# Kernel optimization log

Measured on AMD Instinct MI355X. Metric: run time of the kernel, lower is better.

The kernel has to match this reference:

```python
import jax, jax.numpy as jnp
import numpy as np

N, E, D_IN, H, Z = 50000, 800000, 256, 96, 32
NEG_SLOPE = 0.2  # PyG GATConv default
BN_EPS = 1e-5


def _gat(x, src, dst, W, a, b, n):
    """Single-head GATConv (PyG semantics, self-loops already in src/dst)."""
    h = x @ W                                   # [N, F']
    e = jax.nn.leaky_relu((h @ a[0])[src] + (h @ a[1])[dst], NEG_SLOPE)  # [E]
    m = jax.ops.segment_max(e, dst, num_segments=n)
    ex = jnp.exp(e - m[dst])
    s = jax.ops.segment_sum(ex, dst, num_segments=n)
    alpha = ex / s[dst]                         # softmax over incoming edges
    out = jax.ops.segment_sum(alpha[:, None] * h[src], dst, num_segments=n)
    return out + b


def _bn(x, g, b):
    # BatchNorm1d in training mode: biased batch stats over nodes
    mu = jnp.mean(x, axis=0)
    v = jnp.var(x, axis=0)
    return g * (x - mu) / jnp.sqrt(v + BN_EPS) + b


def setup_inputs() -> dict:
    key = jax.random.key(0)
    ks = jax.random.split(key, 32)
    inp = {}
    inp["x"] = jax.random.normal(ks[0], (N, D_IN), jnp.float32)
    inp["edge_index"] = jax.random.randint(ks[1], (2, E), 0, N)
    inp["eps"] = jax.random.normal(ks[2], (N, Z), jnp.float32)

    def xav(k, di, do):
        s = float(np.sqrt(2.0 / (di + do)))
        return jax.random.normal(k, (di, do), jnp.float32) * s

    layers = [("enc1", D_IN, H), ("enc2", H, H), ("mu", H, Z), ("lv", H, Z),
              ("dec1", Z, H), ("dec2", H, H), ("out", H, D_IN)]
    ki = 3
    for nm, di, do in layers:
        inp[nm + "_W"] = xav(ks[ki], di, do)
        inp[nm + "_a"] = jax.random.normal(ks[ki + 1], (2, do), jnp.float32) * 0.1
        inp[nm + "_b"] = jnp.zeros((do,), jnp.float32)
        ki += 2
    for nm in ["bne1", "bne2", "bnd1", "bnd2"]:
        inp[nm + "_g"] = jnp.ones((H,), jnp.float32)
        inp[nm + "_b"] = jnp.zeros((H,), jnp.float32)
    return inp


def reference(x, edge_index, eps,
              enc1_W, enc1_a, enc1_b, enc2_W, enc2_a, enc2_b,
              mu_W, mu_a, mu_b, lv_W, lv_a, lv_b,
              dec1_W, dec1_a, dec1_b, dec2_W, dec2_a, dec2_b,
              out_W, out_a, out_b,
              bne1_g, bne1_b, bne2_g, bne2_b, bnd1_g, bnd1_b, bnd2_g, bnd2_b):
    n = x.shape[0]
    loop = jnp.arange(n)
    src = jnp.concatenate([edge_index[0], loop])  # add self-loops (GAT default)
    dst = jnp.concatenate([edge_index[1], loop])

    # ---- GraphEncoder ----
    h0 = jax.nn.relu(_bn(_gat(x, src, dst, enc1_W, enc1_a, enc1_b, n), bne1_g, bne1_b))
    h1 = jax.nn.relu(_bn(_gat(h0, src, dst, enc2_W, enc2_a, enc2_b, n), bne2_g, bne2_b))
    h = h1 + h0  # residual from layer 0
    q_m = _gat(h, src, dst, mu_W, mu_a, mu_b, n)
    q_s = _gat(h, src, dst, lv_W, lv_a, lv_b, n)
    std = jax.nn.softplus(q_s) + 1e-6
    q_z = q_m + std * eps  # rsample

    # ---- GraphDecoder ----
    d0 = jax.nn.relu(_bn(_gat(q_z, src, dst, dec1_W, dec1_a, dec1_b, n), bnd1_g, bnd1_b))
    d1 = jax.nn.relu(_bn(_gat(d0, src, dst, dec2_W, dec2_a, dec2_b, n), bnd2_g, bnd2_b))
    d = d1 + d0
    recon = jax.nn.softmax(_gat(d, src, dst, out_W, out_a, out_b, n), axis=-1)
    return q_z, q_m, q_s, recon
```

## Files before the change

kernel.cpp:

```cpp
#include <hip/hip_runtime.h>
#include <math.h>

#define NN 50000
#define EE 800000
#define D_IN 256
#define HDIM 96
#define ZDIM 32
#define MAXD 64
#define GFILL 1661
#define MGRID 782
#define CDIV(a,b) (((a)+(b)-1)/(b))

typedef unsigned int uint;
typedef unsigned short ushort;
typedef __bf16 bf16x8 __attribute__((ext_vector_type(8)));
typedef float f32x4 __attribute__((ext_vector_type(4)));

struct BNP { const float* sc; const float* sh; };

__device__ __forceinline__ ushort f2b(float f) {
  uint x = __float_as_uint(f);
  return (ushort)((x + 0x7fffu + ((x >> 16) & 1u)) >> 16);
}
__device__ __forceinline__ uint pack2(float a, float b) {
  return (uint)f2b(a) | ((uint)f2b(b) << 16);
}
__device__ __forceinline__ float blo(uint u) { return __uint_as_float(u << 16); }
__device__ __forceinline__ float bhi(uint u) { return __uint_as_float(u & 0xffff0000u); }
__device__ __forceinline__ float lrelu(float v) { return v > 0.f ? v : 0.2f * v; }
__device__ __forceinline__ float bnval(const BNP& bn, int f, float x) {
  return fmaxf(fmaf(bn.sc[f], x, bn.sh[f]), 0.f);
}

struct PrepArgs { const float* W[7]; const float* a[7]; };

__global__ void k_prep(PrepArgs p, ushort* __restrict__ wt, float* __restrict__ avb,
                       int* __restrict__ zbase, int zcount) {
  const int SDin[6]  = {256, 96, 96, 32, 96, 96};
  const int SDout[6] = {96, 96, 64, 96, 96, 256};
  const int SL[6]    = {0, 1, 2, 4, 5, 6};
  const int SWoff[6] = {0, 24576, 33792, 39936, 43008, 52224};
  int y = blockIdx.y;
  if (y < 6) {
    int Din = SDin[y], Dout = SDout[y];
    int n = Din * Dout;
    ushort* wo = wt + SWoff[y];
    if (y == 2) {
      const float* W2 = p.W[2];
      const float* W3 = p.W[3];
      for (int o = blockIdx.x * 256 + threadIdx.x; o < n; o += 96 * 256) {
        int c = o / Din, k = o % Din;
        float w = (c < 32) ? W2[(size_t)k * 32 + c] : W3[(size_t)k * 32 + (c - 32)];
        wo[o] = f2b(w);
      }
    } else {
      const float* W = p.W[SL[y]];
      for (int o = blockIdx.x * 256 + threadIdx.x; o < n; o += 96 * 256) {
        int c = o / Din, k = o % Din;
        wo[o] = f2b(W[(size_t)k * Dout + c]);
      }
    }
  } else if (y == 6) {
    int wave = (blockIdx.x * 256 + threadIdx.x) >> 6;
    int lane = threadIdx.x & 63;
    for (int row = wave; row < 128; row += 96 * 4) {
      int l = (row < 32) ? 4 : 6;
      int k = (row < 32) ? row : row - 32;
      int Dout = (l == 4) ? 96 : 256;
      const float* W = p.W[l];
      const float* a = p.a[l];
      float s0 = 0.f, s1 = 0.f;
      for (int c = lane; c < Dout; c += 64) {
        float w = W[(size_t)k * Dout + c];
        s0 = fmaf(w, a[c], s0);
        s1 = fmaf(w, a[Dout + c], s1);
      }
      for (int o = 32; o > 0; o >>= 1) {
        s0 += __shfl_down(s0, o);
        s1 += __shfl_down(s1, o);
      }
      if (lane == 0) {
        if (l == 4) { avb[k] = s0; avb[32 + k] = s1; }
        else { avb[64 + k] = s0; avb[160 + k] = s1; }
      }
    }
  } else {
    for (int i = blockIdx.x * 256 + threadIdx.x; i < zcount; i += 96 * 256)
      zbase[i] = 0;
  }
}

template<int DIN, int DOUT, int AMODE, bool BF16_OUT, bool ADD_BIAS, int EPI>
__device__ __forceinline__ void mfma_body(
    int bid, const void* __restrict__ A1, const void* __restrict__ A2, BNP bn1, BNP bn2,
    const ushort* __restrict__ Wt, const float* __restrict__ bias,
    void* __restrict__ outp, const float* __restrict__ aA, const float* __restrict__ aB,
    float* __restrict__ el, float* __restrict__ er,
    float2* __restrict__ elp, float2* __restrict__ erp) {
  constexpr int NT = DOUT / 16;
  constexpr int KS = DIN / 32;
  const int lane = threadIdx.x & 63;
  const int wv = threadIdx.x >> 6;
  const int row0 = bid * 64 + wv * 16;
  const int cl = lane & 15;
  const int g = lane >> 4;
  const int arow = min(row0 + cl, NN - 1);
  f32x4 acc[NT];
#pragma unroll
  for (int t = 0; t < NT; t++) acc[t] = (f32x4){0.f, 0.f, 0.f, 0.f};
#pragma unroll
  for (int ks = 0; ks < KS; ks++) {
    bf16x8 af;
    if constexpr (AMODE == 0) {
      af = *(const bf16x8*)((const ushort*)A1 + (size_t)arow * DIN + ks * 32 + g * 8);
    } else if constexpr (AMODE == 1) {
      const float* Af = (const float*)A1 + (size_t)arow * DIN + ks * 32 + g * 8;
      float4 lo = *(const float4*)Af;
      float4 hi = *(const float4*)(Af + 4);
      union { uint4 u; bf16x8 v; } cvt;
      cvt.u.x = pack2(lo.x, lo.y); cvt.u.y = pack2(lo.z, lo.w);
      cvt.u.z = pack2(hi.x, hi.y); cvt.u.w = pack2(hi.z, hi.w);
      af = cvt.v;
    } else {
      const float* p1 = (const float*)A1 + (size_t)arow * DIN + ks * 32 + g * 8;
      const float* p2 = (const float*)A2 + (size_t)arow * DIN + ks * 32 + g * 8;
      const int f0 = ks * 32 + g * 8;
      float v[8];
#pragma unroll
      for (int j = 0; j < 8; j++) {
        float t = bnval(bn1, f0 + j, p1[j]);
        if constexpr (AMODE == 3) t += bnval(bn2, f0 + j, p2[j]);
        v[j] = t;
      }
      union { uint4 u; bf16x8 b8; } cv;
      cv.u.x = pack2(v[0], v[1]); cv.u.y = pack2(v[2], v[3]);
      cv.u.z = pack2(v[4], v[5]); cv.u.w = pack2(v[6], v[7]);
      af = cv.b8;
    }
#pragma unroll
    for (int t = 0; t < NT; t++) {
      bf16x8 bf = *(const bf16x8*)(Wt + (size_t)(t * 16 + cl) * DIN + ks * 32 + g * 8);
      acc[t] = __builtin_amdgcn_mfma_f32_16x16x32_bf16(af, bf, acc[t], 0, 0, 0);
    }
  }
  if constexpr (EPI == 1) {
#pragma unroll
    for (int r = 0; r < 4; r++) {
      float l0 = 0.f, l1 = 0.f;
#pragma unroll
      for (int t = 0; t < NT; t++) {
        float w0 = aA[t * 16 + cl], w1 = aA[DOUT + t * 16 + cl];
        l0 = fmaf(acc[t][r], w0, l0);
        l1 = fmaf(acc[t][r], w1, l1);
      }
#pragma unroll
      for (int m = 1; m < 16; m <<= 1) {
        l0 += __shfl_xor(l0, m);
        l1 += __shfl_xor(l1, m);
      }
      int row = row0 + g * 4 + r;
      if (cl == 0 && row < NN) { el[row] = l0; er[row] = l1; }
    }
  }
  if constexpr (EPI == 2) {
#pragma unroll
    for (int r = 0; r < 4; r++) {
      float m0 = 0.f, m1 = 0.f, v0 = 0.f, v1 = 0.f;
#pragma unroll
      for (int t = 0; t < 2; t++) {
        int c = t * 16 + cl;
        m0 = fmaf(acc[t][r], aA[c], m0);
        m1 = fmaf(acc[t][r], aA[32 + c], m1);
        v0 = fmaf(acc[t + 2][r], aB[c], v0);
        v1 = fmaf(acc[t + 2][r], aB[32 + c], v1);
      }
#pragma unroll
      for (int m = 1; m < 16; m <<= 1) {
        m0 += __shfl_xor(m0, m); m1 += __shfl_xor(m1, m);
        v0 += __shfl_xor(v0, m); v1 += __shfl_xor(v1, m);
      }
      int row = row0 + g * 4 + r;
      if (cl == 0 && row < NN) {
        elp[row] = make_float2(m0, v0);
        erp[row] = make_float2(m1, v1);
      }
    }
  }
  if constexpr (ADD_BIAS) {
#pragma unroll
    for (int t = 0; t < NT; t++) {
      float bv = bias[t * 16 + cl];
#pragma unroll
      for (int r = 0; r < 4; r++) acc[t][r] += bv;
    }
  }
  if constexpr (EPI == 3) {
    float mx[4], sm[4];
#pragma unroll
    for (int r = 0; r < 4; r++) mx[r] = -3.4e38f;
#pragma unroll
    for (int t = 0; t < NT; t++)
#pragma unroll
      for (int r = 0; r < 4; r++) mx[r] = fmaxf(mx[r], acc[t][r]);
#pragma unroll
    for (int r = 0; r < 4; r++) {
#pragma unroll
      for (int msk = 1; msk < 16; msk <<= 1)
        mx[r] = fmaxf(mx[r], __shfl_xor(mx[r], msk));
      sm[r] = 0.f;
    }
#pragma unroll
    for (int t = 0; t < NT; t++)
#pragma unroll
      for (int r = 0; r < 4; r++) { acc[t][r] = expf(acc[t][r] - mx[r]); sm[r] += acc[t][r]; }
#pragma unroll
    for (int r = 0; r < 4; r++) {
#pragma unroll
      for (int msk = 1; msk < 16; msk <<= 1) sm[r] += __shfl_xor(sm[r], msk);
      sm[r] = 1.f / sm[r];
    }
#pragma unroll
    for (int t = 0; t < NT; t++)
#pragma unroll
      for (int r = 0; r < 4; r++) acc[t][r] *= sm[r];
  }
#pragma unroll
  for (int r = 0; r < 4; r++) {
    int grow = row0 + g * 4 + r;
    if (grow >= NN) continue;
    if constexpr (BF16_OUT) {
      ushort* o = (ushort*)outp + (size_t)grow * DOUT + cl;
#pragma unroll
      for (int t = 0; t < NT; t++) o[t * 16] = f2b(acc[t][r]);
    } else {
      float* o = (float*)outp + (size_t)grow * DOUT + cl;
#pragma unroll
      for (int t = 0; t < NT; t++) o[t * 16] = acc[t][r];
    }
  }
}

template<int DIN, int DOUT, int AMODE, bool BF16_OUT, bool ADD_BIAS, int EPI>
__global__ __launch_bounds__(256) void k_mfma(
    const void* __restrict__ A1, const void* __restrict__ A2, BNP bn1, BNP bn2,
    const ushort* __restrict__ Wt, const float* __restrict__ bias,
    void* __restrict__ outp, const float* __restrict__ aA, const float* __restrict__ aB,
    float* __restrict__ el, float* __restrict__ er,
    float2* __restrict__ elp, float2* __restrict__ erp) {
  mfma_body<DIN, DOUT, AMODE, BF16_OUT, ADD_BIAS, EPI>(
      blockIdx.x, A1, A2, bn1, bn2, Wt, bias, outp, aA, aB, el, er, elp, erp);
}

__global__ __launch_bounds__(256) void k_fill_gemm(
    const int* __restrict__ eidx, int* __restrict__ pos, ushort* __restrict__ srcs,
    const float* __restrict__ x, const ushort* __restrict__ Wt,
    ushort* __restrict__ hbf, const float* __restrict__ aA,
    float* __restrict__ el, float* __restrict__ er) {
  if (blockIdx.x < GFILL) {
    const int tot = EE + NN;
    int base = blockIdx.x * 512 + threadIdx.x;
#pragma unroll
    for (int j = 0; j < 2; j++) {
      int e = base + j * 256;
      if (e < tot) {
        int s, d;
        if (e < EE) { s = eidx[e]; d = eidx[EE + e]; }
        else { s = e - EE; d = s; }
        int p = atomicAdd(&pos[d], 1);
        if (p < MAXD) srcs[d * MAXD + p] = (ushort)s;
      }
    }
  } else {
    BNP bz{nullptr, nullptr};
    mfma_body<256, 96, 1, true, false, 1>(
        blockIdx.x - GFILL, x, nullptr, bz, bz, Wt, nullptr, hbf, aA, nullptr,
        el, er, nullptr, nullptr);
  }
}

template<int D, bool BF16O, bool STATS>
__global__ __launch_bounds__(256) void k_agg1(
    const ushort* __restrict__ hb, const float* __restrict__ el,
    const float* __restrict__ er, const int* __restrict__ dcnt,
    const ushort* __restrict__ srcs, const float* __restrict__ bias,
    void* __restrict__ out, float* __restrict__ sbuck) {
  constexpr int LPN = (D <= 32) ? 32 : 64;
  constexpr int NPB = 256 / LPN;
  constexpr int NU = D / 2;
  const int tid = threadIdx.x;
  const int slot = tid / LPN;
  const int ln = tid % LPN;
  const int i = blockIdx.x * NPB + slot;
  const int beg = i * MAXD;
  const int deg = min(dcnt[i], MAXD);
  const int end = beg + deg;
  const float eri = er[i];
  const uint* h32 = (const uint*)hb;
  __shared__ float s_al[256];
  __shared__ uint s_of[256];
  float v0 = -3.4e38f;
  int sv0 = 0;
  if (ln < deg) { sv0 = srcs[beg + ln]; v0 = lrelu(el[sv0] + eri); }
  float m = v0;
  for (int c = beg + LPN; c < end; c += LPN) {
    int e = c + ln;
    if (e < end) m = fmaxf(m, lrelu(el[srcs[e]] + eri));
  }
  for (int o = LPN / 2; o; o >>= 1) m = fmaxf(m, __shfl_xor(m, o, LPN));
  float s = (ln < deg) ? expf(v0 - m) : 0.f;
  for (int c = beg + LPN; c < end; c += LPN) {
    int e = c + ln;
    if (e < end) s += expf(lrelu(el[srcs[e]] + eri) - m);
  }
  for (int o = LPN / 2; o; o >>= 1) s += __shfl_xor(s, o, LPN);
  const float inv = 1.0f / s;
  float acc0 = 0.f, acc1 = 0.f;
  if (ln < deg) { s_al[tid] = expf(v0 - m) * inv; s_of[tid] = (uint)sv0 * NU; }
  const int base = slot * LPN;
  int nv = min(LPN, deg);
  if (ln < NU) {
    int t = 0;
    for (; t + 8 <= nv; t += 8) {
      uint o0 = s_of[base + t],     o1 = s_of[base + t + 1];
      uint o2 = s_of[base + t + 2], o3 = s_of[base + t + 3];
      uint o4 = s_of[base + t + 4], o5 = s_of[base + t + 5];
      uint o6 = s_of[base + t + 6], o7 = s_of[base + t + 7];
      uint u0 = h32[o0 + ln], u1 = h32[o1 + ln], u2 = h32[o2 + ln], u3 = h32[o3 + ln];
      uint u4 = h32[o4 + ln], u5 = h32[o5 + ln], u6 = h32[o6 + ln], u7 = h32[o7 + ln];
      float a0 = s_al[base + t],     a1 = s_al[base + t + 1];
      float a2 = s_al[base + t + 2], a3 = s_al[base + t + 3];
      float a4 = s_al[base + t + 4], a5 = s_al[base + t + 5];
      float a6 = s_al[base + t + 6], a7 = s_al[base + t + 7];
      acc0 = fmaf(a0, blo(u0), acc0); acc1 = fmaf(a0, bhi(u0), acc1);
      acc0 = fmaf(a1, blo(u1), acc0); acc1 = fmaf(a1, bhi(u1), acc1);
      acc0 = fmaf(a2, blo(u2), acc0); acc1 = fmaf(a2, bhi(u2), acc1);
      acc0 = fmaf(a3, blo(u3), acc0); acc1 = fmaf(a3, bhi(u3), acc1);
      acc0 = fmaf(a4, blo(u4), acc0); acc1 = fmaf(a4, bhi(u4), acc1);
      acc0 = fmaf(a5, blo(u5), acc0); acc1 = fmaf(a5, bhi(u5), acc1);
      acc0 = fmaf(a6, blo(u6), acc0); acc1 = fmaf(a6, bhi(u6), acc1);
      acc0 = fmaf(a7, blo(u7), acc0); acc1 = fmaf(a7, bhi(u7), acc1);
    }
    for (; t + 4 <= nv; t += 4) {
      uint o0 = s_of[base + t],     o1 = s_of[base + t + 1];
      uint o2 = s_of[base + t + 2], o3 = s_of[base + t + 3];
      uint u0 = h32[o0 + ln], u1 = h32[o1 + ln], u2 = h32[o2 + ln], u3 = h32[o3 + ln];
      float a0 = s_al[base + t],     a1 = s_al[base + t + 1];
      float a2 = s_al[base + t + 2], a3 = s_al[base + t + 3];
      acc0 = fmaf(a0, blo(u0), acc0); acc1 = fmaf(a0, bhi(u0), acc1);
      acc0 = fmaf(a1, blo(u1), acc0); acc1 = fmaf(a1, bhi(u1), acc1);
      acc0 = fmaf(a2, blo(u2), acc0); acc1 = fmaf(a2, bhi(u2), acc1);
      acc0 = fmaf(a3, blo(u3), acc0); acc1 = fmaf(a3, bhi(u3), acc1);
    }
    for (; t < nv; t++) {
      float a = s_al[base + t];
      uint u = h32[s_of[base + t] + ln];
      acc0 = fmaf(a, blo(u), acc0);
      acc1 = fmaf(a, bhi(u), acc1);
    }
  }
  for (int c = beg + LPN; c < end; c += LPN) {
    int e = c + ln;
    if (e < end) {
      int sv = srcs[e];
      s_al[tid] = expf(lrelu(el[sv] + eri) - m) * inv;
      s_of[tid] = (uint)sv * NU;
    }
    int nv2 = min(LPN, end - c);
    if (ln < NU) {
      for (int t = 0; t < nv2; t++) {
        float a = s_al[base + t];
        uint u = h32[s_of[base + t] + ln];
        acc0 = fmaf(a, blo(u), acc0);
        acc1 = fmaf(a, bhi(u), acc1);
      }
    }
  }
  float o0 = 0.f, o1 = 0.f;
  if (ln < NU) {
    float b0 = bias ? bias[2 * ln] : 0.f;
    float b1 = bias ? bias[2 * ln + 1] : 0.f;
    o0 = acc0 + b0;
    o1 = acc1 + b1;
    if constexpr (BF16O) {
      ((uint*)out)[(size_t)i * NU + ln] = pack2(o0, o1);
    } else {
      ((float2*)out)[(size_t)i * NU + ln] = make_float2(o0, o1);
    }
  }
  if constexpr (STATS) {
    __shared__ float s_val[4][96];
    if (ln < NU) {
      s_val[slot][2 * ln] = o0;
      s_val[slot][2 * ln + 1] = o1;
    }
    __syncthreads();
    if (tid < 96) {
      float su = 0.f, sq = 0.f;
#pragma unroll
      for (int s2 = 0; s2 < 4; s2++) {
        float v = s_val[s2][tid];
        su += v;
        sq = fmaf(v, v, sq);
      }
      float* bk = sbuck + (blockIdx.x & 63) * 192;
      atomicAdd(&bk[tid], su);
      atomicAdd(&bk[96 + tid], sq);
    }
  }
}

__global__ void k_bnred(const float* __restrict__ sbuck, int nb,
                        const float* __restrict__ g, const float* __restrict__ b,
                        float* __restrict__ sc, float* __restrict__ sh) {
  int f = threadIdx.x;
  if (f >= 96) return;
  float su = 0.f, sq = 0.f;
  for (int j = 0; j < nb; j++) {
    su += sbuck[j * 192 + f];
    sq += sbuck[j * 192 + 96 + f];
  }
  float mu = su * (1.0f / NN);
  float va = sq * (1.0f / NN) - mu * mu;
  float scale = g[f] * rsqrtf(va + 1e-5f);
  sc[f] = scale;
  sh[f] = fmaf(-scale, mu, b[f]);
}

__global__ __launch_bounds__(256) void k_aggmulv(
    const ushort* __restrict__ hb, const float2* __restrict__ elp,
    const float2* __restrict__ erp, const int* __restrict__ dcnt,
    const ushort* __restrict__ srcs, const float* __restrict__ bmu,
    const float* __restrict__ blv, float* __restrict__ qm, float* __restrict__ qs,
    const float* __restrict__ eps, float* __restrict__ qz,
    ushort* __restrict__ qzbf, const float* __restrict__ av4,
    float* __restrict__ el, float* __restrict__ er) {
  const int tid = threadIdx.x;
  const int slot = tid >> 5;
  const int ln = tid & 31;
  const int i = blockIdx.x * 8 + slot;
  if (i >= NN) return;
  const int beg = i * MAXD;
  const int deg = min(dcnt[i], MAXD);
  const int end = beg + deg;
  const float2 eri = erp[i];
  const uint* h32 = (const uint*)hb;
  __shared__ float s_am[256];
  __shared__ float s_av[256];
  __shared__ uint s_of[256];
  float v0m = -3.4e38f, v0l = -3.4e38f;
  int sv0 = 0;
  if (ln < deg) {
    sv0 = srcs[beg + ln];
    float2 p = elp[sv0];
    v0m = lrelu(p.x + eri.x);
    v0l = lrelu(p.y + eri.y);
  }
  float mm = v0m, ml = v0l;
  for (int c = beg + 32; c < end; c += 32) {
    int e = c + ln;
    if (e < end) {
      float2 p = elp[srcs[e]];
      mm = fmaxf(mm, lrelu(p.x + eri.x));
      ml = fmaxf(ml, lrelu(p.y + eri.y));
    }
  }
  for (int o = 16; o; o >>= 1) {
    mm = fmaxf(mm, __shfl_xor(mm, o, 32));
    ml = fmaxf(ml, __shfl_xor(ml, o, 32));
  }
  float sm = 0.f, sl = 0.f;
  if (ln < deg) { sm = expf(v0m - mm); sl = expf(v0l - ml); }
  for (int c = beg + 32; c < end; c += 32) {
    int e = c + ln;
    if (e < end) {
      float2 p = elp[srcs[e]];
      sm += expf(lrelu(p.x + eri.x) - mm);
      sl += expf(lrelu(p.y + eri.y) - ml);
    }
  }
  for (int o = 16; o; o >>= 1) {
    sm += __shfl_xor(sm, o, 32);
    sl += __shfl_xor(sl, o, 32);
  }
  const float invm = 1.0f / sm, invl = 1.0f / sl;
  float acc0 = 0.f, acc1 = 0.f;
  if (ln < deg) {
    s_am[tid] = expf(v0m - mm) * invm;
    s_av[tid] = expf(v0l - ml) * invl;
    s_of[tid] = (uint)sv0 * 32;
  }
  const int base = slot * 32;
  const float* s_sel = (ln < 16) ? s_am : s_av;
  int nv = min(32, deg);
  int t = 0;
  for (; t + 4 <= nv; t += 4) {
    uint o0 = s_of[base + t],     o1 = s_of[base + t + 1];
    uint o2 = s_of[base + t + 2], o3 = s_of[base + t + 3];
    uint u0 = h32[o0 + ln], u1 = h32[o1 + ln], u2 = h32[o2 + ln], u3 = h32[o3 + ln];
    float a0 = s_sel[base + t],     a1 = s_sel[base + t + 1];
    float a2 = s_sel[base + t + 2], a3 = s_sel[base + t + 3];
    acc0 = fmaf(a0, blo(u0), acc0); acc1 = fmaf(a0, bhi(u0), acc1);
    acc0 = fmaf(a1, blo(u1), acc0); acc1 = fmaf(a1, bhi(u1), acc1);
    acc0 = fmaf(a2, blo(u2), acc0); acc1 = fmaf(a2, bhi(u2), acc1);
    acc0 = fmaf(a3, blo(u3), acc0); acc1 = fmaf(a3, bhi(u3), acc1);
  }
  for (; t < nv; t++) {
    float a = s_sel[base + t];
    uint u = h32[s_of[base + t] + ln];
    acc0 = fmaf(a, blo(u), acc0);
    acc1 = fmaf(a, bhi(u), acc1);
  }
  for (int c = beg + 32; c < end; c += 32) {
    int e = c + ln;
    if (e < end) {
      int sv = srcs[e];
      float2 p = elp[sv];
      s_am[tid] = expf(lrelu(p.x + eri.x) - mm) * invm;
      s_av[tid] = expf(lrelu(p.y + eri.y) - ml) * invl;
      s_of[tid] = (uint)sv * 32;
    }
    int nv2 = min(32, end - c);
    for (int tt = 0; tt < nv2; tt++) {
      float a = s_sel[base + tt];
      uint u = h32[s_of[base + tt] + ln];
      acc0 = fmaf(a, blo(u), acc0);
      acc1 = fmaf(a, bhi(u), acc1);
    }
  }
  float b0 = (ln < 16) ? bmu[2 * ln] : blv[2 * (ln - 16)];
  float b1 = (ln < 16) ? bmu[2 * ln + 1] : blv[2 * (ln - 16) + 1];
  float o0 = acc0 + b0, o1 = acc1 + b1;
  if (ln < 16) ((float2*)qm)[(size_t)i * 16 + ln] = make_float2(o0, o1);
  else ((float2*)qs)[(size_t)i * 16 + (ln - 16)] = make_float2(o0, o1);
  float q0 = __shfl_xor(o0, 16, 32);
  float q1 = __shfl_xor(o1, 16, 32);
  if (ln < 16) {
    float2 ep = ((const float2*)eps)[(size_t)i * 16 + ln];
    float sp0 = fmaxf(q0, 0.f) + log1pf(expf(-fabsf(q0))) + 1e-6f;
    float sp1 = fmaxf(q1, 0.f) + log1pf(expf(-fabsf(q1))) + 1e-6f;
    float z0 = fmaf(sp0, ep.x, o0);
    float z1 = fmaf(sp1, ep.y, o1);
    ((float2*)qz)[(size_t)i * 16 + ln] = make_float2(z0, z1);
    ((uint*)qzbf)[(size_t)i * 16 + ln] = pack2(z0, z1);
    float d0 = z0 * av4[2 * ln] + z1 * av4[2 * ln + 1];
    float d1 = z0 * av4[32 + 2 * ln] + z1 * av4[32 + 2 * ln + 1];
    for (int o = 8; o; o >>= 1) {
      d0 += __shfl_xor(d0, o, 16);
      d1 += __shfl_xor(d1, o, 16);
    }
    if (ln == 0) { el[i] = d0; er[i] = d1; }
  }
}

__global__ void k_bn_stats(const float* __restrict__ x, float* __restrict__ sums,
                           float* __restrict__ sumsq) {
  int f = threadIdx.x;
  float s = 0.f, q = 0.f;
  for (int r = blockIdx.x; r < NN; r += gridDim.x) {
    float v = x[(size_t)r * HDIM + f];
    s += v;
    q = fmaf(v, v, q);
  }
  atomicAdd(&sums[f], s);
  atomicAdd(&sumsq[f], q);
}

__global__ __launch_bounds__(256) void k_bn_dual(
    const float* __restrict__ xA, BNP bnA, const float* __restrict__ xB, BNP bnB,
    ushort* __restrict__ outbf, const float* __restrict__ av, const float* __restrict__ bv,
    float* __restrict__ el, float* __restrict__ er) {
  int w = (blockIdx.x * 256 + threadIdx.x) >> 6;
  int ln = threadIdx.x & 63;
  if (w >= NN) return;
  const size_t base = (size_t)w * HDIM;
  float v1 = bnval(bnA, ln, xA[base + ln]) + bnval(bnB, ln, xB[base + ln]);
  float v2 = 0.f;
  if (ln < 32) {
    int f = 64 + ln;
    v2 = bnval(bnA, f, xA[base + f]) + bnval(bnB, f, xB[base + f]);
  }
  outbf[base + ln] = f2b(v1);
  if (ln < 32) outbf[base + 64 + ln] = f2b(v2);
  float d0 = v1 * av[ln], d1 = v1 * bv[ln];
  if (ln < 32) { d0 = fmaf(v2, av[64 + ln], d0); d1 = fmaf(v2, bv[64 + ln], d1); }
  for (int o = 32; o > 0; o >>= 1) {
    d0 += __shfl_down(d0, o);
    d1 += __shfl_down(d1, o);
  }
  if (ln == 0) { el[w] = d0; er[w] = d1; }
}

extern "C" void kernel_launch(void* const* d_in, const int* in_sizes, int n_in,
                              void* d_out, int out_size, void* d_ws, size_t ws_size,
                              hipStream_t stream) {
  const float* x    = (const float*)d_in[0];
  const int*   eidx = (const int*)d_in[1];
  const float* eps  = (const float*)d_in[2];
  const float *W[7], *Aa[7], *Bb[7];
  for (int l = 0; l < 7; l++) {
    W[l]  = (const float*)d_in[3 + 3 * l];
    Aa[l] = (const float*)d_in[4 + 3 * l];
    Bb[l] = (const float*)d_in[5 + 3 * l];
  }
  const float* bng[4] = {(const float*)d_in[24], (const float*)d_in[26],
                         (const float*)d_in[28], (const float*)d_in[30]};
  const float* bnb[4] = {(const float*)d_in[25], (const float*)d_in[27],
                         (const float*)d_in[29], (const float*)d_in[31]};

  size_t off_b = 0;
  auto alloc = [&](size_t bytes) -> void* {
    void* p = (char*)d_ws + off_b;
    off_b = (off_b + bytes + 255) & ~(size_t)255;
    return p;
  };
  ushort* hbf   = (ushort*)alloc((size_t)NN * HDIM * 2);
  ushort* sh2   = (ushort*)alloc((size_t)NN * HDIM * 2);
  float* bufB   = (float*)alloc((size_t)NN * HDIM * 4);
  float* bufD   = (float*)alloc((size_t)NN * HDIM * 4);
  ushort* qzbf  = (ushort*)alloc((size_t)NN * ZDIM * 2);
  float* el     = (float*)alloc((size_t)NN * 4);
  float* er     = (float*)alloc((size_t)NN * 4);
  float2* elp   = (float2*)alloc((size_t)NN * 8);
  float2* erp   = (float2*)alloc((size_t)NN * 8);
  const int ZCNT = NN + 3 * 64 * 192 + 192;
  char* zregion = (char*)alloc((size_t)ZCNT * 4);
  int* dcnt     = (int*)zregion;
  float* sb0    = (float*)(dcnt + NN);
  float* sb1    = sb0 + 64 * 192;
  float* sb2    = sb1 + 64 * 192;
  float* st2    = sb2 + 64 * 192;
  ushort* srcs  = (ushort*)alloc((size_t)NN * MAXD * 2);
  ushort* wt    = (ushort*)alloc((size_t)76800 * 2);
  float* avb    = (float*)alloc((size_t)256 * 4);
  float* scsh   = (float*)alloc((size_t)4 * 192 * 4);
  (void)alloc(65536);

  float* qz    = (float*)d_out;
  float* qm    = qz + (size_t)NN * ZDIM;
  float* qs    = qm + (size_t)NN * ZDIM;
  float* recon = qs + (size_t)NN * ZDIM;

  const int wgrid = CDIV(NN * 64, 256);
  const int SW[6] = {0, 24576, 33792, 39936, 43008, 52224};

  BNP bnp[4];
  for (int i = 0; i < 4; i++) bnp[i] = BNP{scsh + i * 192, scsh + i * 192 + 96};
  BNP bz{nullptr, nullptr};

  PrepArgs pa;
  for (int l = 0; l < 7; l++) { pa.W[l] = W[l]; pa.a[l] = Aa[l]; }
  k_prep<<<dim3(96, 8), 256, 0, stream>>>(pa, wt, avb, dcnt, ZCNT);

  k_fill_gemm<<<GFILL + MGRID, 256, 0, stream>>>(eidx, dcnt, srcs,
                                                 x, wt + SW[0], hbf, Aa[0], el, er);

  k_agg1<96, false, true><<<CDIV(NN, 4), 256, 0, stream>>>(hbf, el, er, dcnt, srcs,
                                                           Bb[0], bufB, sb0);
  k_bnred<<<1, 96, 0, stream>>>(sb0, 64, bng[0], bnb[0], scsh, scsh + 96);

  k_mfma<96, 96, 2, true, false, 1><<<MGRID, 256, 0, stream>>>(
      bufB, nullptr, bnp[0], bz, wt + SW[1], nullptr, hbf, Aa[1], nullptr, el, er, nullptr, nullptr);
  k_agg1<96, false, true><<<CDIV(NN, 4), 256, 0, stream>>>(hbf, el, er, dcnt, srcs,
                                                           Bb[1], bufD, sb1);
  k_bnred<<<1, 96, 0, stream>>>(sb1, 64, bng[1], bnb[1], scsh + 192, scsh + 192 + 96);

  k_mfma<96, 64, 3, true, false, 2><<<MGRID, 256, 0, stream>>>(
      bufD, bufB, bnp[1], bnp[0], wt + SW[2], nullptr, hbf, Aa[2], Aa[3],
      nullptr, nullptr, elp, erp);
  k_aggmulv<<<CDIV(NN, 8), 256, 0, stream>>>(hbf, elp, erp, dcnt, srcs, Bb[2], Bb[3],
                                             qm, qs, eps, qz, qzbf, avb, el, er);

  k_agg1<32, true, false><<<CDIV(NN, 8), 256, 0, stream>>>(qzbf, el, er, dcnt, srcs,
                                                           nullptr, hbf, nullptr);
  k_mfma<32, 96, 0, false, true, 0><<<MGRID, 256, 0, stream>>>(
      hbf, nullptr, bz, bz, wt + SW[3], Bb[4], bufB, nullptr, nullptr,
      nullptr, nullptr, nullptr, nullptr);
  k_bn_stats<<<512, 96, 0, stream>>>(bufB, st2, st2 + 96);
  k_bnred<<<1, 96, 0, stream>>>(st2, 1, bng[2], bnb[2], scsh + 384, scsh + 384 + 96);

  k_mfma<96, 96, 2, true, false, 1><<<MGRID, 256, 0, stream>>>(
      bufB, nullptr, bnp[2], bz, wt + SW[4], nullptr, hbf, Aa[5], nullptr, el, er, nullptr, nullptr);
  k_agg1<96, false, true><<<CDIV(NN, 4), 256, 0, stream>>>(hbf, el, er, dcnt, srcs,
                                                           Bb[5], bufD, sb2);
  k_bnred<<<1, 96, 0, stream>>>(sb2, 64, bng[3], bnb[3], scsh + 576, scsh + 576 + 96);

  k_bn_dual<<<wgrid, 256, 0, stream>>>(bufD, bnp[3], bufB, bnp[2], sh2,
                                       avb + 64, avb + 160, el, er);

  k_agg1<96, true, false><<<CDIV(NN, 4), 256, 0, stream>>>(sh2, el, er, dcnt, srcs,
                                                           nullptr, hbf, nullptr);
  k_mfma<96, 256, 0, false, true, 3><<<MGRID, 256, 0, stream>>>(
      hbf, nullptr, bz, bz, wt + SW[5], Bb[6], recon, nullptr, nullptr,
      nullptr, nullptr, nullptr, nullptr);
}
```

Measured before the change: 463.6 us.

## Bucket edges by destination before CSR fill and fold BN reductions into consumers

The edge-to-CSR fill is split into two passes. The first partitions edges into 64 destination-range buckets, using shared-memory histograms. The second does the per-node atomic slot fill bucket by bucket, for better atomic locality, while the first GEMM runs alongside. The standalone BatchNorm reduction and stats kernels are removed. Scale/shift are now recomputed per block from the bucketed partial sums inside the consuming GEMM and bn_dual kernels, and the dec1 GEMM accumulates its own column stats in its epilogue. This cuts several tiny serial launches and a full re-read of the decoder activation, at the cost of an extra edge pass, a bucket buffer with a fixed capacity that could overflow, and redundant per-block reductions.

Result: faster. 405.9 us (-12.5%).

```diff
diff --git a/kernel.cpp b/kernel.cpp
--- a/kernel.cpp
+++ b/kernel.cpp
@@ -3,11 +3,13 @@
 
 #define NN 50000
 #define EE 800000
-#define D_IN 256
 #define HDIM 96
 #define ZDIM 32
 #define MAXD 64
-#define GFILL 1661
+#define NBUK 64
+#define BCAP 16384
+#define BMUL 1341
+#define NBB 512
 #define MGRID 782
 #define CDIV(a,b) (((a)+(b)-1)/(b))
 
@@ -16,8 +18,6 @@
 typedef __bf16 bf16x8 __attribute__((ext_vector_type(8)));
 typedef float f32x4 __attribute__((ext_vector_type(4)));
 
-struct BNP { const float* sc; const float* sh; };
-
 __device__ __forceinline__ ushort f2b(float f) {
   uint x = __float_as_uint(f);
   return (ushort)((x + 0x7fffu + ((x >> 16) & 1u)) >> 16);
@@ -28,8 +28,24 @@
 __device__ __forceinline__ float blo(uint u) { return __uint_as_float(u << 16); }
 __device__ __forceinline__ float bhi(uint u) { return __uint_as_float(u & 0xffff0000u); }
 __device__ __forceinline__ float lrelu(float v) { return v > 0.f ? v : 0.2f * v; }
-__device__ __forceinline__ float bnval(const BNP& bn, int f, float x) {
-  return fmaxf(fmaf(bn.sc[f], x, bn.sh[f]), 0.f);
+
+__device__ __forceinline__ void red_scsh(const float* __restrict__ sb,
+                                         const float* __restrict__ g,
+                                         const float* __restrict__ b,
+                                         float* s_c, float* s_h, int tid) {
+  if (tid < 96) {
+    float su = 0.f, sq = 0.f;
+#pragma unroll 8
+    for (int j = 0; j < NBUK; j++) {
+      su += sb[j * 192 + tid];
+      sq += sb[j * 192 + 96 + tid];
+    }
+    float mu = su * (1.0f / NN);
+    float va = sq * (1.0f / NN) - mu * mu;
+    float sc = g[tid] * rsqrtf(va + 1e-5f);
+    s_c[tid] = sc;
+    s_h[tid] = fmaf(-sc, mu, b[tid]);
+  }
 }
 
 struct PrepArgs { const float* W[7]; const float* a[7]; };
@@ -90,21 +106,66 @@
   }
 }
 
-template<int DIN, int DOUT, int AMODE, bool BF16_OUT, bool ADD_BIAS, int EPI>
+__global__ __launch_bounds__(256) void k_partA(const int* __restrict__ eidx,
+                                               int* __restrict__ bcnt,
+                                               uint* __restrict__ barr) {
+  __shared__ int hist[NBUK];
+  __shared__ int hbase[NBUK];
+  const int tot = EE + NN;
+  const int tid = threadIdx.x;
+  int base = blockIdx.x * 512 + tid;
+  if (tid < NBUK) hist[tid] = 0;
+  __syncthreads();
+  int dv[2], sv[2], bk[2], ofs[2];
+  bool ok[2];
+#pragma unroll
+  for (int j = 0; j < 2; j++) {
+    int e = base + j * 256;
+    ok[j] = e < tot;
+    dv[j] = sv[j] = bk[j] = ofs[j] = 0;
+    if (ok[j]) {
+      if (e < EE) { sv[j] = eidx[e]; dv[j] = eidx[EE + e]; }
+      else { sv[j] = dv[j] = e - EE; }
+      bk[j] = (dv[j] * BMUL) >> 20;
+      ofs[j] = atomicAdd(&hist[bk[j]], 1);
+    }
+  }
+  __syncthreads();
+  if (tid < NBUK) hbase[tid] = atomicAdd(&bcnt[tid], hist[tid]);
+  __syncthreads();
+#pragma unroll
+  for (int j = 0; j < 2; j++) {
+    if (ok[j]) {
+      int w = hbase[bk[j]] + ofs[j];
+      if (w < BCAP) barr[bk[j] * BCAP + w] = ((uint)dv[j] << 16) | (uint)sv[j];
+    }
+  }
+}
+
+template<int DIN, int DOUT, int AMODE, bool BF16_OUT, bool ADD_BIAS, int EPI, bool STATS>
 __device__ __forceinline__ void mfma_body(
-    int bid, const void* __restrict__ A1, const void* __restrict__ A2, BNP bn1, BNP bn2,
+    int bid, const void* __restrict__ A1, const void* __restrict__ A2,
+    const float* __restrict__ sbA, const float* __restrict__ gA, const float* __restrict__ bA,
+    const float* __restrict__ sbB, const float* __restrict__ gB, const float* __restrict__ bB,
     const ushort* __restrict__ Wt, const float* __restrict__ bias,
     void* __restrict__ outp, const float* __restrict__ aA, const float* __restrict__ aB,
     float* __restrict__ el, float* __restrict__ er,
-    float2* __restrict__ elp, float2* __restrict__ erp) {
+    float2* __restrict__ elp, float2* __restrict__ erp, float* __restrict__ sbout) {
   constexpr int NT = DOUT / 16;
   constexpr int KS = DIN / 32;
-  const int lane = threadIdx.x & 63;
-  const int wv = threadIdx.x >> 6;
+  const int tid = threadIdx.x;
+  const int lane = tid & 63;
+  const int wv = tid >> 6;
   const int row0 = bid * 64 + wv * 16;
   const int cl = lane & 15;
   const int g = lane >> 4;
   const int arow = min(row0 + cl, NN - 1);
+  __shared__ float s_c1[96], s_h1[96], s_c2[96], s_h2[96];
+  if constexpr (AMODE >= 2) {
+    red_scsh(sbA, gA, bA, s_c1, s_h1, tid);
+    if constexpr (AMODE == 3) red_scsh(sbB, gB, bB, s_c2, s_h2, tid);
+    __syncthreads();
+  }
   f32x4 acc[NT];
 #pragma unroll
   for (int t = 0; t < NT; t++) acc[t] = (f32x4){0.f, 0.f, 0.f, 0.f};
@@ -128,8 +189,9 @@
       float v[8];
 #pragma unroll
       for (int j = 0; j < 8; j++) {
-        float t = bnval(bn1, f0 + j, p1[j]);
-        if constexpr (AMODE == 3) t += bnval(bn2, f0 + j, p2[j]);
+        float t = fmaxf(fmaf(s_c1[f0 + j], p1[j], s_h1[f0 + j]), 0.f);
+        if constexpr (AMODE == 3)
+          t += fmaxf(fmaf(s_c2[f0 + j], p2[j], s_h2[f0 + j]), 0.f);
         v[j] = t;
       }
       union { uint4 u; bf16x8 b8; } cv;
@@ -194,6 +256,31 @@
       for (int r = 0; r < 4; r++) acc[t][r] += bv;
     }
   }
+  if constexpr (STATS) {
+    __shared__ float s_su[96], s_sq[96];
+    if (tid < 96) { s_su[tid] = 0.f; s_sq[tid] = 0.f; }
+    __syncthreads();
+#pragma unroll
+    for (int t = 0; t < NT; t++) {
+      float su = 0.f, sq = 0.f;
+#pragma unroll
+      for (int r = 0; r < 4; r++) {
+        if (row0 + g * 4 + r < NN) {
+          float v = acc[t][r];
+          su += v;
+          sq = fmaf(v, v, sq);
+        }
+      }
+      atomicAdd(&s_su[t * 16 + cl], su);
+      atomicAdd(&s_sq[t * 16 + cl], sq);
+    }
+    __syncthreads();
+    if (tid < 96) {
+      float* bk = sbout + (bid & 63) * 192;
+      atomicAdd(&bk[tid], s_su[tid]);
+      atomicAdd(&bk[96 + tid], s_sq[tid]);
+    }
+  }
   if constexpr (EPI == 3) {
     float mx[4], sm[4];
 #pragma unroll
@@ -240,41 +327,42 @@
   }
 }
 
-template<int DIN, int DOUT, int AMODE, bool BF16_OUT, bool ADD_BIAS, int EPI>
+template<int DIN, int DOUT, int AMODE, bool BF16_OUT, bool ADD_BIAS, int EPI, bool STATS>
 __global__ __launch_bounds__(256) void k_mfma(
-    const void* __restrict__ A1, const void* __restrict__ A2, BNP bn1, BNP bn2,
+    const void* __restrict__ A1, const void* __restrict__ A2,
+    const float* __restrict__ sbA, const float* __restrict__ gA, const float* __restrict__ bA,
+    const float* __restrict__ sbB, const float* __restrict__ gB, const float* __restrict__ bB,
     const ushort* __restrict__ Wt, const float* __restrict__ bias,
     void* __restrict__ outp, const float* __restrict__ aA, const float* __restrict__ aB,
     float* __restrict__ el, float* __restrict__ er,
-    float2* __restrict__ elp, float2* __restrict__ erp) {
-  mfma_body<DIN, DOUT, AMODE, BF16_OUT, ADD_BIAS, EPI>(
-      blockIdx.x, A1, A2, bn1, bn2, Wt, bias, outp, aA, aB, el, er, elp, erp);
-}
-
-__global__ __launch_bounds__(256) void k_fill_gemm(
-    const int* __restrict__ eidx, int* __restrict__ pos, ushort* __restrict__ srcs,
+    float2* __restrict__ elp, float2* __restrict__ erp, float* __restrict__ sbout) {
+  mfma_body<DIN, DOUT, AMODE, BF16_OUT, ADD_BIAS, EPI, STATS>(
+      blockIdx.x, A1, A2, sbA, gA, bA, sbB, gB, bB, Wt, bias, outp, aA, aB,
+      el, er, elp, erp, sbout);
+}
+
+__global__ __launch_bounds__(256) void k_fatB(
+    const int* __restrict__ bcnt, const uint* __restrict__ barr,
+    int* __restrict__ dcnt, ushort* __restrict__ srcs,
     const float* __restrict__ x, const ushort* __restrict__ Wt,
     ushort* __restrict__ hbf, const float* __restrict__ aA,
     float* __restrict__ el, float* __restrict__ er) {
-  if (blockIdx.x < GFILL) {
-    const int tot = EE + NN;
-    int base = blockIdx.x * 512 + threadIdx.x;
-#pragma unroll
-    for (int j = 0; j < 2; j++) {
-      int e = base + j * 256;
-      if (e < tot) {
-        int s, d;
-        if (e < EE) { s = eidx[e]; d = eidx[EE + e]; }
-        else { s = e - EE; d = s; }
-        int p = atomicAdd(&pos[d], 1);
-        if (p < MAXD) srcs[d * MAXD + p] = (ushort)s;
-      }
+  if (blockIdx.x < NBB) {
+    const int bucket = blockIdx.x & 63;
+    const int j = blockIdx.x >> 6;
+    const int n = min(bcnt[bucket], BCAP);
+    const uint* bp = barr + bucket * BCAP;
+    for (int idx = j * 256 + (int)threadIdx.x; idx < n; idx += 2048) {
+      uint e = bp[idx];
+      int d = (int)(e >> 16);
+      int s = (int)(e & 0xffffu);
+      int p = atomicAdd(&dcnt[d], 1);
+      if (p < MAXD) srcs[d * MAXD + p] = (ushort)s;
     }
   } else {
-    BNP bz{nullptr, nullptr};
-    mfma_body<256, 96, 1, true, false, 1>(
-        blockIdx.x - GFILL, x, nullptr, bz, bz, Wt, nullptr, hbf, aA, nullptr,
-        el, er, nullptr, nullptr);
+    mfma_body<256, 96, 1, true, false, 1, false>(
+        blockIdx.x - NBB, x, nullptr, nullptr, nullptr, nullptr, nullptr, nullptr, nullptr,
+        Wt, nullptr, hbf, aA, nullptr, el, er, nullptr, nullptr, nullptr);
   }
 }
 
@@ -407,23 +495,6 @@
       atomicAdd(&bk[96 + tid], sq);
     }
   }
-}
-
-__global__ void k_bnred(const float* __restrict__ sbuck, int nb,
-                        const float* __restrict__ g, const float* __restrict__ b,
-                        float* __restrict__ sc, float* __restrict__ sh) {
-  int f = threadIdx.x;
-  if (f >= 96) return;
-  float su = 0.f, sq = 0.f;
-  for (int j = 0; j < nb; j++) {
-    su += sbuck[j * 192 + f];
-    sq += sbuck[j * 192 + 96 + f];
-  }
-  float mu = su * (1.0f / NN);
-  float va = sq * (1.0f / NN) - mu * mu;
-  float scale = g[f] * rsqrtf(va + 1e-5f);
-  sc[f] = scale;
-  sh[f] = fmaf(-scale, mu, b[f]);
 }
 
 __global__ __launch_bounds__(256) void k_aggmulv(
@@ -552,42 +623,42 @@
   }
 }
 
-__global__ void k_bn_stats(const float* __restrict__ x, float* __restrict__ sums,
-                           float* __restrict__ sumsq) {
-  int f = threadIdx.x;
-  float s = 0.f, q = 0.f;
-  for (int r = blockIdx.x; r < NN; r += gridDim.x) {
-    float v = x[(size_t)r * HDIM + f];
-    s += v;
-    q = fmaf(v, v, q);
-  }
-  atomicAdd(&sums[f], s);
-  atomicAdd(&sumsq[f], q);
-}
-
 __global__ __launch_bounds__(256) void k_bn_dual(
-    const float* __restrict__ xA, BNP bnA, const float* __restrict__ xB, BNP bnB,
+    const float* __restrict__ xA, const float* __restrict__ sbA,
+    const float* __restrict__ gA, const float* __restrict__ bA,
+    const float* __restrict__ xB, const float* __restrict__ sbB,
+    const float* __restrict__ gB, const float* __restrict__ bB,
     ushort* __restrict__ outbf, const float* __restrict__ av, const float* __restrict__ bv,
     float* __restrict__ el, float* __restrict__ er) {
-  int w = (blockIdx.x * 256 + threadIdx.x) >> 6;
-  int ln = threadIdx.x & 63;
-  if (w >= NN) return;
-  const size_t base = (size_t)w * HDIM;
-  float v1 = bnval(bnA, ln, xA[base + ln]) + bnval(bnB, ln, xB[base + ln]);
-  float v2 = 0.f;
-  if (ln < 32) {
-    int f = 64 + ln;
-    v2 = bnval(bnA, f, xA[base + f]) + bnval(bnB, f, xB[base + f]);
-  }
-  outbf[base + ln] = f2b(v1);
-  if (ln < 32) outbf[base + 64 + ln] = f2b(v2);
-  float d0 = v1 * av[ln], d1 = v1 * bv[ln];
-  if (ln < 32) { d0 = fmaf(v2, av[64 + ln], d0); d1 = fmaf(v2, bv[64 + ln], d1); }
-  for (int o = 32; o > 0; o >>= 1) {
-    d0 += __shfl_down(d0, o);
-    d1 += __shfl_down(d1, o);
-  }
-  if (ln == 0) { el[w] = d0; er[w] = d1; }
+  __shared__ float cA[96], hA[96], cB[96], hB[96];
+  const int tid = threadIdx.x;
+  red_scsh(sbA, gA, bA, cA, hA, tid);
+  red_scsh(sbB, gB, bB, cB, hB, tid);
+  __syncthreads();
+  const int wv = tid >> 6;
+  const int ln = tid & 63;
+  for (int it = 0; it < 16; it++) {
+    int w = blockIdx.x * 64 + it * 4 + wv;
+    if (w >= NN) return;
+    const size_t base = (size_t)w * HDIM;
+    float v1 = fmaxf(fmaf(cA[ln], xA[base + ln], hA[ln]), 0.f) +
+               fmaxf(fmaf(cB[ln], xB[base + ln], hB[ln]), 0.f);
+    float v2 = 0.f;
+    if (ln < 32) {
+      int f = 64 + ln;
+      v2 = fmaxf(fmaf(cA[f], xA[base + f], hA[f]), 0.f) +
+           fmaxf(fmaf(cB[f], xB[base + f], hB[f]), 0.f);
+    }
+    outbf[base + ln] = f2b(v1);
+    if (ln < 32) outbf[base + 64 + ln] = f2b(v2);
+    float d0 = v1 * av[ln], d1 = v1 * bv[ln];
+    if (ln < 32) { d0 = fmaf(v2, av[64 + ln], d0); d1 = fmaf(v2, bv[64 + ln], d1); }
+    for (int o = 32; o > 0; o >>= 1) {
+      d0 += __shfl_down(d0, o);
+      d1 += __shfl_down(d1, o);
+    }
+    if (ln == 0) { el[w] = d0; er[w] = d1; }
+  }
 }
 
 extern "C" void kernel_launch(void* const* d_in, const int* in_sizes, int n_in,
@@ -622,17 +693,18 @@
   float* er     = (float*)alloc((size_t)NN * 4);
   float2* elp   = (float2*)alloc((size_t)NN * 8);
   float2* erp   = (float2*)alloc((size_t)NN * 8);
-  const int ZCNT = NN + 3 * 64 * 192 + 192;
+  const int ZCNT = NN + NBUK + 4 * NBUK * 192;
   char* zregion = (char*)alloc((size_t)ZCNT * 4);
   int* dcnt     = (int*)zregion;
-  float* sb0    = (float*)(dcnt + NN);
-  float* sb1    = sb0 + 64 * 192;
-  float* sb2    = sb1 + 64 * 192;
-  float* st2    = sb2 + 64 * 192;
+  int* bcnt     = dcnt + NN;
+  float* sb0    = (float*)(bcnt + NBUK);
+  float* sb1    = sb0 + NBUK * 192;
+  float* sb2    = sb1 + NBUK * 192;
+  float* sb3    = sb2 + NBUK * 192;
   ushort* srcs  = (ushort*)alloc((size_t)NN * MAXD * 2);
+  uint* barr    = (uint*)alloc((size_t)NBUK * BCAP * 4);
   ushort* wt    = (ushort*)alloc((size_t)76800 * 2);
   float* avb    = (float*)alloc((size_t)256 * 4);
-  float* scsh   = (float*)alloc((size_t)4 * 192 * 4);
   (void)alloc(65536);
 
   float* qz    = (float*)d_out;
@@ -640,56 +712,46 @@
   float* qs    = qm + (size_t)NN * ZDIM;
   float* recon = qs + (size_t)NN * ZDIM;
 
-  const int wgrid = CDIV(NN * 64, 256);
   const int SW[6] = {0, 24576, 33792, 39936, 43008, 52224};
-
-  BNP bnp[4];
-  for (int i = 0; i < 4; i++) bnp[i] = BNP{scsh + i * 192, scsh + i * 192 + 96};
-  BNP bz{nullptr, nullptr};
+  const float* nf = nullptr;
 
   PrepArgs pa;
   for (int l = 0; l < 7; l++) { pa.W[l] = W[l]; pa.a[l] = Aa[l]; }
   k_prep<<<dim3(96, 8), 256, 0, stream>>>(pa, wt, avb, dcnt, ZCNT);
 
-  k_fill_gemm<<<GFILL + MGRID, 256, 0, stream>>>(eidx, dcnt, srcs,
-                                                 x, wt + SW[0], hbf, Aa[0], el, er);
+  k_partA<<<CDIV(EE + NN, 512), 256, 0, stream>>>(eidx, bcnt, barr);
+  k_fatB<<<NBB + MGRID, 256, 0, stream>>>(bcnt, barr, dcnt, srcs,
+                                          x, wt + SW[0], hbf, Aa[0], el, er);
 
   k_agg1<96, false, true><<<CDIV(NN, 4), 256, 0, stream>>>(hbf, el, er, dcnt, srcs,
                                                            Bb[0], bufB, sb0);
-  k_bnred<<<1, 96, 0, stream>>>(sb0, 64, bng[0], bnb[0], scsh, scsh + 96);
-
-  k_mfma<96, 96, 2, true, false, 1><<<MGRID, 256, 0, stream>>>(
-      bufB, nullptr, bnp[0], bz, wt + SW[1], nullptr, hbf, Aa[1], nullptr, el, er, nullptr, nullptr);
+  k_mfma<96, 96, 2, true, false, 1, false><<<MGRID, 256, 0, stream>>>(
+      bufB, nullptr, sb0, bng[0], bnb[0], nf, nf, nf, wt + SW[1], nullptr, hbf,
+      Aa[1], nullptr, el, er, nullptr, nullptr, nullptr);
   k_agg1<96, false, true><<<CDIV(NN, 4), 256, 0, stream>>>(hbf, el, er, dcnt, srcs,
                                                            Bb[1], bufD, sb1);
-  k_bnred<<<1, 96, 0, stream>>>(sb1, 64, bng[1], bnb[1], scsh + 192, scsh + 192 + 96);
-
-  k_mfma<96, 64, 3, true, false, 2><<<MGRID, 256, 0, stream>>>(
-      bufD, bufB, bnp[1], bnp[0], wt + SW[2], nullptr, hbf, Aa[2], Aa[3],
-      nullptr, nullptr, elp, erp);
+  k_mfma<96, 64, 3, true, false, 2, false><<<MGRID, 256, 0, stream>>>(
+      bufD, bufB, sb1, bng[1], bnb[1], sb0, bng[0], bnb[0], wt + SW[2], nullptr, hbf,
+      Aa[2], Aa[3], nullptr, nullptr, elp, erp, nullptr);
   k_aggmulv<<<CDIV(NN, 8), 256, 0, stream>>>(hbf, elp, erp, dcnt, srcs, Bb[2], Bb[3],
                                              qm, qs, eps, qz, qzbf, avb, el, er);
 
   k_agg1<32, true, false><<<CDIV(NN, 8), 256, 0, stream>>>(qzbf, el, er, dcnt, srcs,
                                                            nullptr, hbf, nullptr);
-  k_mfma<32, 96, 0, false, true, 0><<<MGRID, 256, 0, stream>>>(
-      hbf, nullptr, bz, bz, wt + SW[3], Bb[4], bufB, nullptr, nullptr,
-      nullptr, nullptr, nullptr, nullptr);
-  k_bn_stats<<<512, 96, 0, stream>>>(bufB, st2, st2 + 96);
-  k_bnred<<<1, 96, 0, stream>>>(st2, 1, bng[2], bnb[2], scsh + 384, scsh + 384 + 96);
-
-  k_mfma<96, 96, 2, true, false, 1><<<MGRID, 256, 0, stream>>>(
-      bufB, nullptr, bnp[2], bz, wt + SW[4], nullptr, hbf, Aa[5], nullptr, el, er, nullptr, nullptr);
+  k_mfma<32, 96, 0, false, true, 0, true><<<MGRID, 256, 0, stream>>>(
+      hbf, nullptr, nf, nf, nf, nf, nf, nf, wt + SW[3], Bb[4], bufB,
+      nullptr, nullptr, nullptr, nullptr, nullptr, nullptr, sb2);
+  k_mfma<96, 96, 2, true, false, 1, false><<<MGRID, 256, 0, stream>>>(
+      bufB, nullptr, sb2, bng[2], bnb[2], nf, nf, nf, wt + SW[4], nullptr, hbf,
+      Aa[5], nullptr, el, er, nullptr, nullptr, nullptr);
   k_agg1<96, false, true><<<CDIV(NN, 4), 256, 0, stream>>>(hbf, el, er, dcnt, srcs,
-                                                           Bb[5], bufD, sb2);
-  k_bnred<<<1, 96, 0, stream>>>(sb2, 64, bng[3], bnb[3], scsh + 576, scsh + 576 + 96);
-
-  k_bn_dual<<<wgrid, 256, 0, stream>>>(bufD, bnp[3], bufB, bnp[2], sh2,
-                                       avb + 64, avb + 160, el, er);
-
+                                                           Bb[5], bufD, sb3);
+  k_bn_dual<<<MGRID, 256, 0, stream>>>(bufD, sb3, bng[3], bnb[3],
+                                       bufB, sb2, bng[2], bnb[2],
+                                       sh2, avb + 64, avb + 160, el, er);
   k_agg1<96, true, false><<<CDIV(NN, 4), 256, 0, stream>>>(sh2, el, er, dcnt, srcs,
                                                            nullptr, hbf, nullptr);
-  k_mfma<96, 256, 0, false, true, 3><<<MGRID, 256, 0, stream>>>(
-      hbf, nullptr, bz, bz, wt + SW[5], Bb[6], recon, nullptr, nullptr,
-      nullptr, nullptr, nullptr, nullptr);
-}
+  k_mfma<96, 256, 0, false, true, 3, false><<<MGRID, 256, 0, stream>>>(
+      hbf, nullptr, nf, nf, nf, nf, nf, nf, wt + SW[5], Bb[6], recon,
+      nullptr, nullptr, nullptr, nullptr, nullptr, nullptr, nullptr);
+}
```
